# Optimization experiments

Hardware: AMD Instinct MI355X
Metric: run time of the kernel (lower is better)

Reference implementation:

```python
import jax, jax.numpy as jnp
import numpy as np

LAMDA = 0.5

def setup_inputs() -> dict:
    key = jax.random.key(0)
    k1, k2 = jax.random.split(key)
    X_set = jax.random.normal(k1, (8192, 128), dtype=jnp.float32)
    Y_set = jax.random.randint(k2, (8192,), 0, 100, dtype=jnp.int64)
    return {"X_set": X_set, "Y_set": Y_set}

def _pairwise_euclidean(X):
    # X: [N, D] -> D: [N, N] euclidean distances (torch.cdist p=2)
    sq_norms = jnp.sum(X * X, axis=1)  # [N]
    sq = sq_norms[:, None] + sq_norms[None, :] - 2.0 * (X @ X.T)  # [N, N]
    sq = jnp.maximum(sq, 0.0)
    # safe sqrt (zero diagonal) to stay grad-safe under jit
    pos = sq > 0.0
    return jnp.where(pos, jnp.sqrt(jnp.where(pos, sq, 1.0)), 0.0)

def reference(X_set, Y_set):
    X = X_set.reshape(X_set.shape[0], -1)
    D = _pairwise_euclidean(X)  # [N, N]
    same = Y_set[:, None] == Y_set[None, :]  # [N, N] bool
    # Class loop in original == sum of within-class distances (incl. zero diag)
    # minus lamda * sum over all ordered cross-class pairs (each unordered
    # cross pair is counted once for each of its two classes -> full mask).
    pos_sum = jnp.sum(jnp.where(same, D, 0.0))
    neg_sum = jnp.sum(jnp.where(same, 0.0, D))
    return pos_sum - LAMDA * neg_sum
```

## Files before the change

### kernel.cpp

```cpp
#include <hip/hip_runtime.h>

#define N_ROWS 8192
#define DIM    128
#define BM     128
#define NBLK   (N_ROWS / BM)
#define NTRI   (NBLK * (NBLK + 1) / 2)

#define BLOB_PER_RB   65536
#define BLOB_PER_PH   16384

typedef _Float16 half8 __attribute__((ext_vector_type(8)));
typedef float    f32x16 __attribute__((ext_vector_type(16)));

typedef const __attribute__((address_space(1))) unsigned int glb_uint;
typedef __attribute__((address_space(3))) unsigned int lds_uint;

__device__ inline void gload_lds16(const void* g, void* l)
{
    __builtin_amdgcn_global_load_lds((glb_uint*)(uintptr_t)g,
                                     (lds_uint*)(uintptr_t)l, 16, 0, 0);
}

__global__ __launch_bounds__(256)
void prep_tiled(const float* __restrict__ X, char* __restrict__ blob,
                float* __restrict__ norms)
{
    const int t    = blockIdx.x * 256 + threadIdx.x;
    const int ksub = t & 3;
    const int p    = (t >> 2) & 3;
    const int row  = t >> 4;

    const float4* src = (const float4*)(X + (size_t)row * DIM + p * 32 + ksub * 8);
    const float4 v0 = src[0], v1 = src[1];
    const float xs[8] = {v0.x, v0.y, v0.z, v0.w, v1.x, v1.y, v1.z, v1.w};

    half8 h, l;
    float ns = 0.0f;
    #pragma unroll
    for (int i = 0; i < 8; ++i) {
        const float x = xs[i];
        const _Float16 hh = (_Float16)x;
        h[i] = hh;
        l[i] = (_Float16)(x - (float)hh);
        ns = fmaf(x, x, ns);
    }

    const int rb   = row >> 7;
    const int r    = row & 127;
    const int g32  = r >> 5;
    const int q    = ksub >> 1;
    const int slot = (r & 31) + (ksub & 1) * 32;
    char* base = blob + (size_t)rb * BLOB_PER_RB + p * BLOB_PER_PH
               + g32 * 4096 + q * 1024 + slot * 16;
    *(half8*)(base)        = h;
    *(half8*)(base + 2048) = l;

    #pragma unroll
    for (int off = 1; off <= 8; off <<= 1) ns += __shfl_xor(ns, off);
    if ((t & 15) == 0) norms[row] = ns;
}

__global__ __launch_bounds__(256, 4)
void pairsum_mfma(const char* __restrict__ blob, const float* __restrict__ norms,
                  const int* __restrict__ Y, double* __restrict__ gsum)
{
    const int kb = blockIdx.x;
    int bi = (int)((129.0f - sqrtf(fmaf(-8.0f, (float)kb, 129.0f * 129.0f))) * 0.5f);
    while ((bi + 1) * (129 - (bi + 1)) / 2 <= kb) ++bi;
    while (bi * (129 - bi) / 2 > kb) --bi;
    const int bj = bi + (kb - bi * (129 - bi) / 2);
    const int i0 = bi * BM, j0 = bj * BM;

    const int tid  = threadIdx.x;
    const int lane = tid & 63;
    const int w    = tid >> 6;
    const int wy   = w >> 1;
    const int wx   = w & 1;
    const int lr   = lane & 31;
    const int lh   = lane >> 5;

    __shared__ __align__(16) char tile[32768];
    __shared__ float nI[BM], nJ[BM];
    __shared__ int   yI[BM], yJ[BM];
    __shared__ double wsum[4];

    if (tid < BM) { nI[tid] = norms[i0 + tid]; yI[tid] = Y[i0 + tid]; }
    else { const int r = tid & (BM - 1); nJ[r] = norms[j0 + r]; yJ[r] = Y[j0 + r]; }
    __syncthreads();

    const char* Apan = blob + (size_t)bi * BLOB_PER_RB;
    const char* Bpan = blob + (size_t)bj * BLOB_PER_RB;

    f32x16 acc[2][2];
    #pragma unroll
    for (int m = 0; m < 2; ++m)
        #pragma unroll
        for (int n = 0; n < 2; ++n)
            #pragma unroll
            for (int r = 0; r < 16; ++r)
                acc[m][n][r] = 0.0f;

    for (int p = 0; p < 4; ++p) {
        #pragma unroll
        for (int r = 0; r < 4; ++r) {
            gload_lds16(Apan + p * BLOB_PER_PH + r * 4096 + tid * 16,
                        tile + r * 4096 + tid * 16);
            gload_lds16(Bpan + p * BLOB_PER_PH + r * 4096 + tid * 16,
                        tile + 16384 + r * 4096 + tid * 16);
        }
        asm volatile("s_waitcnt vmcnt(0)" ::: "memory");
        __builtin_amdgcn_s_barrier();

        #pragma unroll
        for (int q = 0; q < 2; ++q) {
            half8 ah[2], al[2], bh[2], bl[2];
            #pragma unroll
            for (int m = 0; m < 2; ++m) {
                const int ga = (wy * 2 + m) * 4096 + q * 1024 + lane * 16;
                ah[m] = *(const half8*)(tile + ga);
                al[m] = *(const half8*)(tile + ga + 2048);
                const int gb = 16384 + (wx * 2 + m) * 4096 + q * 1024 + lane * 16;
                bh[m] = *(const half8*)(tile + gb);
                bl[m] = *(const half8*)(tile + gb + 2048);
            }
            #pragma unroll
            for (int m = 0; m < 2; ++m)
                #pragma unroll
                for (int n = 0; n < 2; ++n) {
                    acc[m][n] = __builtin_amdgcn_mfma_f32_32x32x16_f16(ah[m], bh[n], acc[m][n], 0, 0, 0);
                    acc[m][n] = __builtin_amdgcn_mfma_f32_32x32x16_f16(ah[m], bl[n], acc[m][n], 0, 0, 0);
                    acc[m][n] = __builtin_amdgcn_mfma_f32_32x32x16_f16(al[m], bh[n], acc[m][n], 0, 0, 0);
                }
        }
        __builtin_amdgcn_s_barrier();
    }

    float s = 0.0f;
    float nJv[2]; int yJv[2];
    #pragma unroll
    for (int n = 0; n < 2; ++n) {
        const int lj = wx * 64 + n * 32 + lr;
        nJv[n] = nJ[lj]; yJv[n] = yJ[lj];
    }
    #pragma unroll
    for (int m = 0; m < 2; ++m) {
        #pragma unroll
        for (int r = 0; r < 16; ++r) {
            const int rowin = (r & 3) + 8 * (r >> 2) + 4 * lh;
            const int li = wy * 64 + m * 32 + rowin;
            const float ni = nI[li];
            const int   yi = yI[li];
            const int   gi = i0 + li;
            #pragma unroll
            for (int n = 0; n < 2; ++n) {
                const int gj = j0 + wx * 64 + n * 32 + lr;
                float sq = fmaf(-2.0f, acc[m][n][r], ni + nJv[n]);
                sq = fmaxf(sq, 0.0f);
                const float d = __builtin_amdgcn_sqrtf(sq);
                if (gi < gj) s = fmaf((yi == yJv[n]) ? 1.0f : -0.5f, d, s);
            }
        }
    }

    #pragma unroll
    for (int off = 32; off > 0; off >>= 1) s += __shfl_down(s, off);
    if (lane == 0) wsum[w] = (double)s;
    __syncthreads();
    if (tid == 0) atomicAdd(gsum, wsum[0] + wsum[1] + wsum[2] + wsum[3]);
}

__global__ void finalize_kernel(const double* __restrict__ gsum, float* __restrict__ out)
{
    out[0] = (float)(2.0 * gsum[0]);
}

#define LDSPAD 4
#define LDB (BM + LDSPAD)
__global__ __launch_bounds__(256)
void pairsum_valu(const float* __restrict__ X, const int* __restrict__ Y,
                  double* __restrict__ gsum)
{
    const int bj = blockIdx.x, bi = blockIdx.y;
    if (bi > bj) return;
    const int tid = threadIdx.x;
    const int i0 = bi * BM, j0 = bj * BM;
    __shared__ float As[32][LDB], Bs[32][LDB];
    __shared__ float nI[BM], nJ[BM];
    __shared__ int yI[BM], yJ[BM];
    __shared__ double wsum[4];
    {
        const int r = tid & (BM - 1);
        const bool isJ = tid >= BM;
        const int row = (isJ ? j0 : i0) + r;
        const float4* p = (const float4*)(X + (size_t)row * DIM);
        float s = 0.f;
        #pragma unroll
        for (int q = 0; q < DIM / 4; ++q) {
            float4 v = p[q];
            s = fmaf(v.x, v.x, s); s = fmaf(v.y, v.y, s);
            s = fmaf(v.z, v.z, s); s = fmaf(v.w, v.w, s);
        }
        if (isJ) { nJ[r] = s; yJ[r] = Y[row]; }
        else     { nI[r] = s; yI[r] = Y[row]; }
    }
    float dot[8][8];
    #pragma unroll
    for (int m = 0; m < 8; ++m)
        #pragma unroll
        for (int n = 0; n < 8; ++n) dot[m][n] = 0.f;
    const int tx = tid & 15, ty = tid >> 4;
    for (int kc = 0; kc < DIM; kc += 32) {
        __syncthreads();
        #pragma unroll
        for (int p = 0; p < 4; ++p) {
            const int s2 = p * 256 + tid;
            const int row = s2 >> 3, kg = s2 & 7;
            const float4 va = *(const float4*)(X + (size_t)(i0 + row) * DIM + kc + kg * 4);
            const float4 vb = *(const float4*)(X + (size_t)(j0 + row) * DIM + kc + kg * 4);
            As[kg*4+0][row] = va.x; As[kg*4+1][row] = va.y;
            As[kg*4+2][row] = va.z; As[kg*4+3][row] = va.w;
            Bs[kg*4+0][row] = vb.x; Bs[kg*4+1][row] = vb.y;
            Bs[kg*4+2][row] = vb.z; Bs[kg*4+3][row] = vb.w;
        }
        __syncthreads();
        #pragma unroll
        for (int k = 0; k < 32; ++k) {
            float a[8], b[8];
            *(float4*)&a[0] = *(const float4*)&As[k][ty*8];
            *(float4*)&a[4] = *(const float4*)&As[k][ty*8+4];
            *(float4*)&b[0] = *(const float4*)&Bs[k][tx*8];
            *(float4*)&b[4] = *(const float4*)&Bs[k][tx*8+4];
            #pragma unroll
            for (int m = 0; m < 8; ++m)
                #pragma unroll
                for (int n = 0; n < 8; ++n)
                    dot[m][n] = fmaf(a[m], b[n], dot[m][n]);
        }
    }
    float s = 0.f;
    const int ib = ty * 8, jb = tx * 8;
    #pragma unroll
    for (int m = 0; m < 8; ++m) {
        const int gi = i0 + ib + m;
        const float ni = nI[ib + m];
        const int yi = yI[ib + m];
        #pragma unroll
        for (int n = 0; n < 8; ++n) {
            const int gj = j0 + jb + n;
            float sq = fmaf(-2.f, dot[m][n], ni + nJ[jb + n]);
            sq = fmaxf(sq, 0.f);
            const float d = __builtin_amdgcn_sqrtf(sq);
            if (gi < gj) s = fmaf((yi == yJ[jb + n]) ? 1.0f : -0.5f, d, s);
        }
    }
    #pragma unroll
    for (int off = 32; off > 0; off >>= 1) s += __shfl_down(s, off);
    const int lane = tid & 63, wid = tid >> 6;
    if (lane == 0) wsum[wid] = (double)s;
    __syncthreads();
    if (tid == 0) atomicAdd(gsum, wsum[0] + wsum[1] + wsum[2] + wsum[3]);
}

extern "C" void kernel_launch(void* const* d_in, const int* in_sizes, int n_in,
                              void* d_out, int out_size, void* d_ws, size_t ws_size,
                              hipStream_t stream)
{
    const float* X = (const float*)d_in[0];
    const int*   Y = (const int*)d_in[1];
    float* out = (float*)d_out;

    const size_t OFF_BLOB = 64;
    const size_t OFF_NORM = OFF_BLOB + (size_t)NBLK * BLOB_PER_RB;
    const size_t REQ      = OFF_NORM + (size_t)N_ROWS * 4;

    double* gsum = (double*)d_ws;
    hipMemsetAsync(d_ws, 0, sizeof(double), stream);

    if (ws_size >= REQ) {
        char*  blob  = (char*)d_ws + OFF_BLOB;
        float* norms = (float*)((char*)d_ws + OFF_NORM);
        prep_tiled<<<(N_ROWS * 16) / 256, 256, 0, stream>>>(X, blob, norms);
        pairsum_mfma<<<NTRI, 256, 0, stream>>>(blob, norms, Y, gsum);
    } else {
        dim3 grid(NBLK, NBLK);
        pairsum_valu<<<grid, 256, 0, stream>>>(X, Y, gsum);
    }
    finalize_kernel<<<1, 1, 0, stream>>>(gsum, out);
}
```

Measured before the change: 109.2 us.

## Use 256-row tiles with 512-thread blocks and double-buffered LDS K-phases

The MFMA pair-sum kernel now tiles 256x256 row blocks instead of 128x128, using 8 waves per block, each computing a 128x64 sub-tile. The blob layout is re-packed into 8 K-phases of 16 columns, and global-to-LDS loads for the next phase are issued before computing the current one, using two LDS buffers. This halves the number of panel loads per output element and overlaps memory with MFMA. In exchange it uses 64KB of LDS and more accumulator registers, which lowers occupancy, and the triangular grid shrinks to 528 blocks with coarser diagonal waste.

```diff
diff --git a/kernel.cpp b/kernel.cpp
--- a/kernel.cpp
+++ b/kernel.cpp
@@ -1,12 +1,13 @@
 #include <hip/hip_runtime.h>
 
-#define N_ROWS 8192
-#define DIM    128
-#define BM     128
-#define NBLK   (N_ROWS / BM)
-#define NTRI   (NBLK * (NBLK + 1) / 2)
-
-#define BLOB_PER_RB   65536
+#define N_ROWS  8192
+#define DIM     128
+#define BM      256
+#define NPAN    (N_ROWS / BM)
+#define NTRI    (NPAN * (NPAN + 1) / 2)
+#define NPH     8
+
+#define BLOB_PER_RB   131072
 #define BLOB_PER_PH   16384
 
 typedef _Float16 half8 __attribute__((ext_vector_type(8)));
@@ -25,12 +26,13 @@
 void prep_tiled(const float* __restrict__ X, char* __restrict__ blob,
                 float* __restrict__ norms)
 {
-    const int t    = blockIdx.x * 256 + threadIdx.x;
-    const int ksub = t & 3;
-    const int p    = (t >> 2) & 3;
-    const int row  = t >> 4;
-
-    const float4* src = (const float4*)(X + (size_t)row * DIM + p * 32 + ksub * 8);
+    const int t   = blockIdx.x * 256 + threadIdx.x;
+    const int kq  = t & 15;
+    const int p   = kq >> 1;
+    const int ks  = kq & 1;
+    const int row = t >> 4;
+
+    const float4* src = (const float4*)(X + (size_t)row * DIM + kq * 8);
     const float4 v0 = src[0], v1 = src[1];
     const float xs[8] = {v0.x, v0.y, v0.z, v0.w, v1.x, v1.y, v1.z, v1.w};
 
@@ -45,93 +47,105 @@
         ns = fmaf(x, x, ns);
     }
 
-    const int rb   = row >> 7;
-    const int r    = row & 127;
+    const int rb   = row >> 8;
+    const int r    = row & 255;
     const int g32  = r >> 5;
-    const int q    = ksub >> 1;
-    const int slot = (r & 31) + (ksub & 1) * 32;
+    const int slot = (r & 31) + ks * 32;
     char* base = blob + (size_t)rb * BLOB_PER_RB + p * BLOB_PER_PH
-               + g32 * 4096 + q * 1024 + slot * 16;
+               + g32 * 2048 + slot * 16;
     *(half8*)(base)        = h;
-    *(half8*)(base + 2048) = l;
+    *(half8*)(base + 1024) = l;
 
     #pragma unroll
     for (int off = 1; off <= 8; off <<= 1) ns += __shfl_xor(ns, off);
     if ((t & 15) == 0) norms[row] = ns;
 }
 
-__global__ __launch_bounds__(256, 4)
+__global__ __launch_bounds__(512, 2)
 void pairsum_mfma(const char* __restrict__ blob, const float* __restrict__ norms,
                   const int* __restrict__ Y, double* __restrict__ gsum)
 {
     const int kb = blockIdx.x;
-    int bi = (int)((129.0f - sqrtf(fmaf(-8.0f, (float)kb, 129.0f * 129.0f))) * 0.5f);
-    while ((bi + 1) * (129 - (bi + 1)) / 2 <= kb) ++bi;
-    while (bi * (129 - bi) / 2 > kb) --bi;
-    const int bj = bi + (kb - bi * (129 - bi) / 2);
+    int bi = (int)((65.0f - sqrtf(fmaf(-8.0f, (float)kb, 65.0f * 65.0f))) * 0.5f);
+    while ((bi + 1) * (65 - (bi + 1)) / 2 <= kb) ++bi;
+    while (bi * (65 - bi) / 2 > kb) --bi;
+    const int bj = bi + (kb - bi * (65 - bi) / 2);
     const int i0 = bi * BM, j0 = bj * BM;
 
     const int tid  = threadIdx.x;
     const int lane = tid & 63;
     const int w    = tid >> 6;
-    const int wy   = w >> 1;
-    const int wx   = w & 1;
+    const int wy   = w >> 2;
+    const int wx   = w & 3;
     const int lr   = lane & 31;
     const int lh   = lane >> 5;
 
-    __shared__ __align__(16) char tile[32768];
+    __shared__ __align__(16) char tile[65536];
     __shared__ float nI[BM], nJ[BM];
     __shared__ int   yI[BM], yJ[BM];
-    __shared__ double wsum[4];
+    __shared__ double wsum[8];
 
     if (tid < BM) { nI[tid] = norms[i0 + tid]; yI[tid] = Y[i0 + tid]; }
-    else { const int r = tid & (BM - 1); nJ[r] = norms[j0 + r]; yJ[r] = Y[j0 + r]; }
+    else { const int r = tid - BM; nJ[r] = norms[j0 + r]; yJ[r] = Y[j0 + r]; }
     __syncthreads();
 
     const char* Apan = blob + (size_t)bi * BLOB_PER_RB;
     const char* Bpan = blob + (size_t)bj * BLOB_PER_RB;
 
-    f32x16 acc[2][2];
-    #pragma unroll
-    for (int m = 0; m < 2; ++m)
+    auto STAGE = [&](int p, int s) {
+        #pragma unroll
+        for (int r = 0; r < 2; ++r) {
+            gload_lds16(Apan + p * BLOB_PER_PH + r * 8192 + tid * 16,
+                        tile + s * 32768 + r * 8192 + tid * 16);
+            gload_lds16(Bpan + p * BLOB_PER_PH + r * 8192 + tid * 16,
+                        tile + s * 32768 + 16384 + r * 8192 + tid * 16);
+        }
+    };
+
+    f32x16 acc[4][2];
+    #pragma unroll
+    for (int m = 0; m < 4; ++m)
         #pragma unroll
         for (int n = 0; n < 2; ++n)
             #pragma unroll
             for (int r = 0; r < 16; ++r)
                 acc[m][n][r] = 0.0f;
 
-    for (int p = 0; p < 4; ++p) {
-        #pragma unroll
-        for (int r = 0; r < 4; ++r) {
-            gload_lds16(Apan + p * BLOB_PER_PH + r * 4096 + tid * 16,
-                        tile + r * 4096 + tid * 16);
-            gload_lds16(Bpan + p * BLOB_PER_PH + r * 4096 + tid * 16,
-                        tile + 16384 + r * 4096 + tid * 16);
-        }
-        asm volatile("s_waitcnt vmcnt(0)" ::: "memory");
-        __builtin_amdgcn_s_barrier();
-
-        #pragma unroll
-        for (int q = 0; q < 2; ++q) {
-            half8 ah[2], al[2], bh[2], bl[2];
+    STAGE(0, 0);
+    asm volatile("s_waitcnt vmcnt(0)" ::: "memory");
+    __builtin_amdgcn_s_barrier();
+    __builtin_amdgcn_sched_barrier(0);
+
+    #pragma unroll
+    for (int p = 0; p < NPH; ++p) {
+        if (p + 1 < NPH) STAGE(p + 1, (p + 1) & 1);
+
+        const char* Ab = tile + (p & 1) * 32768;
+        const char* Bb = Ab + 16384;
+        half8 ah[4], al[4], bh[2], bl[2];
+        #pragma unroll
+        for (int m = 0; m < 4; ++m) {
+            const int ga = (wy * 4 + m) * 2048 + lane * 16;
+            ah[m] = *(const half8*)(Ab + ga);
+            al[m] = *(const half8*)(Ab + ga + 1024);
+        }
+        #pragma unroll
+        for (int n = 0; n < 2; ++n) {
+            const int gb = (wx * 2 + n) * 2048 + lane * 16;
+            bh[n] = *(const half8*)(Bb + gb);
+            bl[n] = *(const half8*)(Bb + gb + 1024);
+        }
+        #pragma unroll
+        for (int m = 0; m < 4; ++m)
             #pragma unroll
-            for (int m = 0; m < 2; ++m) {
-                const int ga = (wy * 2 + m) * 4096 + q * 1024 + lane * 16;
-                ah[m] = *(const half8*)(tile + ga);
-                al[m] = *(const half8*)(tile + ga + 2048);
-                const int gb = 16384 + (wx * 2 + m) * 4096 + q * 1024 + lane * 16;
-                bh[m] = *(const half8*)(tile + gb);
-                bl[m] = *(const half8*)(tile + gb + 2048);
+            for (int n = 0; n < 2; ++n) {
+                acc[m][n] = __builtin_amdgcn_mfma_f32_32x32x16_f16(ah[m], bh[n], acc[m][n], 0, 0, 0);
+                acc[m][n] = __builtin_amdgcn_mfma_f32_32x32x16_f16(ah[m], bl[n], acc[m][n], 0, 0, 0);
+                acc[m][n] = __builtin_amdgcn_mfma_f32_32x32x16_f16(al[m], bh[n], acc[m][n], 0, 0, 0);
             }
-            #pragma unroll
-            for (int m = 0; m < 2; ++m)
-                #pragma unroll
-                for (int n = 0; n < 2; ++n) {
-                    acc[m][n] = __builtin_amdgcn_mfma_f32_32x32x16_f16(ah[m], bh[n], acc[m][n], 0, 0, 0);
-                    acc[m][n] = __builtin_amdgcn_mfma_f32_32x32x16_f16(ah[m], bl[n], acc[m][n], 0, 0, 0);
-                    acc[m][n] = __builtin_amdgcn_mfma_f32_32x32x16_f16(al[m], bh[n], acc[m][n], 0, 0, 0);
-                }
-        }
+
+        asm volatile("s_waitcnt vmcnt(0) lgkmcnt(0)" ::: "memory");
+        __builtin_amdgcn_sched_barrier(0);
         __builtin_amdgcn_s_barrier();
     }
 
@@ -143,11 +157,11 @@
         nJv[n] = nJ[lj]; yJv[n] = yJ[lj];
     }
     #pragma unroll
-    for (int m = 0; m < 2; ++m) {
+    for (int m = 0; m < 4; ++m) {
         #pragma unroll
         for (int r = 0; r < 16; ++r) {
             const int rowin = (r & 3) + 8 * (r >> 2) + 4 * lh;
-            const int li = wy * 64 + m * 32 + rowin;
+            const int li = wy * 128 + m * 32 + rowin;
             const float ni = nI[li];
             const int   yi = yI[li];
             const int   gi = i0 + li;
@@ -166,7 +180,12 @@
     for (int off = 32; off > 0; off >>= 1) s += __shfl_down(s, off);
     if (lane == 0) wsum[w] = (double)s;
     __syncthreads();
-    if (tid == 0) atomicAdd(gsum, wsum[0] + wsum[1] + wsum[2] + wsum[3]);
+    if (tid == 0) {
+        double t2 = 0.0;
+        #pragma unroll
+        for (int q = 0; q < 8; ++q) t2 += wsum[q];
+        atomicAdd(gsum, t2);
+    }
 }
 
 __global__ void finalize_kernel(const double* __restrict__ gsum, float* __restrict__ out)
@@ -174,8 +193,9 @@
     out[0] = (float)(2.0 * gsum[0]);
 }
 
+#define FBM 128
 #define LDSPAD 4
-#define LDB (BM + LDSPAD)
+#define LDB (FBM + LDSPAD)
 __global__ __launch_bounds__(256)
 void pairsum_valu(const float* __restrict__ X, const int* __restrict__ Y,
                   double* __restrict__ gsum)
@@ -183,14 +203,14 @@
     const int bj = blockIdx.x, bi = blockIdx.y;
     if (bi > bj) return;
     const int tid = threadIdx.x;
-    const int i0 = bi * BM, j0 = bj * BM;
+    const int i0 = bi * FBM, j0 = bj * FBM;
     __shared__ float As[32][LDB], Bs[32][LDB];
-    __shared__ float nI[BM], nJ[BM];
-    __shared__ int yI[BM], yJ[BM];
+    __shared__ float nI[FBM], nJ[FBM];
+    __shared__ int yI[FBM], yJ[FBM];
     __shared__ double wsum[4];
     {
-        const int r = tid & (BM - 1);
-        const bool isJ = tid >= BM;
+        const int r = tid & (FBM - 1);
+        const bool isJ = tid >= FBM;
         const int row = (isJ ? j0 : i0) + r;
         const float4* p = (const float4*)(X + (size_t)row * DIM);
         float s = 0.f;
@@ -270,7 +290,7 @@
     float* out = (float*)d_out;
 
     const size_t OFF_BLOB = 64;
-    const size_t OFF_NORM = OFF_BLOB + (size_t)NBLK * BLOB_PER_RB;
+    const size_t OFF_NORM = OFF_BLOB + (size_t)NPAN * BLOB_PER_RB;
     const size_t REQ      = OFF_NORM + (size_t)N_ROWS * 4;
 
     double* gsum = (double*)d_ws;
@@ -280,9 +300,9 @@
         char*  blob  = (char*)d_ws + OFF_BLOB;
         float* norms = (float*)((char*)d_ws + OFF_NORM);
         prep_tiled<<<(N_ROWS * 16) / 256, 256, 0, stream>>>(X, blob, norms);
-        pairsum_mfma<<<NTRI, 256, 0, stream>>>(blob, norms, Y, gsum);
+        pairsum_mfma<<<NTRI, 512, 0, stream>>>(blob, norms, Y, gsum);
     } else {
-        dim3 grid(NBLK, NBLK);
+        dim3 grid(N_ROWS / FBM, N_ROWS / FBM);
         pairsum_valu<<<grid, 256, 0, stream>>>(X, Y, gsum);
     }
     finalize_kernel<<<1, 1, 0, stream>>>(gsum, out);
```

Result: slower. 113.8 us (+4.2%).

## Drop LDS staging, fold zeroing and finalize into compute kernels

Applied to the files above, without the earlier changes.

The MFMA kernel now reads fragments straight from global memory (the pre-tiled blob) instead of staging panels through LDS with barriers. The memset is moved into the prep kernel, and the finalize launch is replaced by a last-block-done counter pattern. This cuts two launches and all per-phase barriers, at the cost of uncoalesced-ish direct global loads per wave and redundant A/B fetches across waves relying on cache.

```diff
diff --git a/kernel.cpp b/kernel.cpp
--- a/kernel.cpp
+++ b/kernel.cpp
@@ -6,29 +6,24 @@
 #define NBLK   (N_ROWS / BM)
 #define NTRI   (NBLK * (NBLK + 1) / 2)
 
-#define BLOB_PER_RB   65536
-#define BLOB_PER_PH   16384
+#define BLOB_PER_RB 65536
+#define BLOB_PER_PH 16384
 
 typedef _Float16 half8 __attribute__((ext_vector_type(8)));
 typedef float    f32x16 __attribute__((ext_vector_type(16)));
 
-typedef const __attribute__((address_space(1))) unsigned int glb_uint;
-typedef __attribute__((address_space(3))) unsigned int lds_uint;
-
-__device__ inline void gload_lds16(const void* g, void* l)
-{
-    __builtin_amdgcn_global_load_lds((glb_uint*)(uintptr_t)g,
-                                     (lds_uint*)(uintptr_t)l, 16, 0, 0);
-}
-
 __global__ __launch_bounds__(256)
 void prep_tiled(const float* __restrict__ X, char* __restrict__ blob,
-                float* __restrict__ norms)
+                float* __restrict__ norms, double* __restrict__ gsum,
+                unsigned int* __restrict__ counter)
 {
     const int t    = blockIdx.x * 256 + threadIdx.x;
-    const int ksub = t & 3;
-    const int p    = (t >> 2) & 3;
+    const int kq   = t & 15;
+    const int p    = kq >> 2;
+    const int ksub = kq & 3;
     const int row  = t >> 4;
+
+    if (t == 0) { *gsum = 0.0; *counter = 0u; }
 
     const float4* src = (const float4*)(X + (size_t)row * DIM + p * 32 + ksub * 8);
     const float4 v0 = src[0], v1 = src[1];
@@ -47,7 +42,7 @@
 
     const int rb   = row >> 7;
     const int r    = row & 127;
-    const int g32  = r >> 5;
+    const int g32  = (r >> 5) & 3;
     const int q    = ksub >> 1;
     const int slot = (r & 31) + (ksub & 1) * 32;
     char* base = blob + (size_t)rb * BLOB_PER_RB + p * BLOB_PER_PH
@@ -62,7 +57,8 @@
 
 __global__ __launch_bounds__(256, 4)
 void pairsum_mfma(const char* __restrict__ blob, const float* __restrict__ norms,
-                  const int* __restrict__ Y, double* __restrict__ gsum)
+                  const int* __restrict__ Y, double* __restrict__ gsum,
+                  unsigned int* __restrict__ counter, float* __restrict__ out)
 {
     const int kb = blockIdx.x;
     int bi = (int)((129.0f - sqrtf(fmaf(-8.0f, (float)kb, 129.0f * 129.0f))) * 0.5f);
@@ -79,7 +75,6 @@
     const int lr   = lane & 31;
     const int lh   = lane >> 5;
 
-    __shared__ __align__(16) char tile[32768];
     __shared__ float nI[BM], nJ[BM];
     __shared__ int   yI[BM], yJ[BM];
     __shared__ double wsum[4];
@@ -100,28 +95,21 @@
             for (int r = 0; r < 16; ++r)
                 acc[m][n][r] = 0.0f;
 
+    #pragma unroll
     for (int p = 0; p < 4; ++p) {
-        #pragma unroll
-        for (int r = 0; r < 4; ++r) {
-            gload_lds16(Apan + p * BLOB_PER_PH + r * 4096 + tid * 16,
-                        tile + r * 4096 + tid * 16);
-            gload_lds16(Bpan + p * BLOB_PER_PH + r * 4096 + tid * 16,
-                        tile + 16384 + r * 4096 + tid * 16);
-        }
-        asm volatile("s_waitcnt vmcnt(0)" ::: "memory");
-        __builtin_amdgcn_s_barrier();
-
         #pragma unroll
         for (int q = 0; q < 2; ++q) {
             half8 ah[2], al[2], bh[2], bl[2];
             #pragma unroll
             for (int m = 0; m < 2; ++m) {
-                const int ga = (wy * 2 + m) * 4096 + q * 1024 + lane * 16;
-                ah[m] = *(const half8*)(tile + ga);
-                al[m] = *(const half8*)(tile + ga + 2048);
-                const int gb = 16384 + (wx * 2 + m) * 4096 + q * 1024 + lane * 16;
-                bh[m] = *(const half8*)(tile + gb);
-                bl[m] = *(const half8*)(tile + gb + 2048);
+                const char* a = Apan + p * BLOB_PER_PH + (wy * 2 + m) * 4096
+                              + q * 1024 + lane * 16;
+                ah[m] = *(const half8*)a;
+                al[m] = *(const half8*)(a + 2048);
+                const char* b = Bpan + p * BLOB_PER_PH + (wx * 2 + m) * 4096
+                              + q * 1024 + lane * 16;
+                bh[m] = *(const half8*)b;
+                bl[m] = *(const half8*)(b + 2048);
             }
             #pragma unroll
             for (int m = 0; m < 2; ++m)
@@ -132,7 +120,6 @@
                     acc[m][n] = __builtin_amdgcn_mfma_f32_32x32x16_f16(al[m], bh[n], acc[m][n], 0, 0, 0);
                 }
         }
-        __builtin_amdgcn_s_barrier();
     }
 
     float s = 0.0f;
@@ -166,7 +153,16 @@
     for (int off = 32; off > 0; off >>= 1) s += __shfl_down(s, off);
     if (lane == 0) wsum[w] = (double)s;
     __syncthreads();
-    if (tid == 0) atomicAdd(gsum, wsum[0] + wsum[1] + wsum[2] + wsum[3]);
+    if (tid == 0) {
+        atomicAdd(gsum, wsum[0] + wsum[1] + wsum[2] + wsum[3]);
+        __threadfence();
+        const unsigned int old = atomicAdd(counter, 1u);
+        if (old == NTRI - 1) {
+            __threadfence();
+            const double tot = atomicAdd(gsum, 0.0);
+            out[0] = (float)(2.0 * tot);
+        }
+    }
 }
 
 __global__ void finalize_kernel(const double* __restrict__ gsum, float* __restrict__ out)
@@ -273,17 +269,18 @@
     const size_t OFF_NORM = OFF_BLOB + (size_t)NBLK * BLOB_PER_RB;
     const size_t REQ      = OFF_NORM + (size_t)N_ROWS * 4;
 
-    double* gsum = (double*)d_ws;
-    hipMemsetAsync(d_ws, 0, sizeof(double), stream);
+    double*       gsum    = (double*)d_ws;
+    unsigned int* counter = (unsigned int*)((char*)d_ws + 8);
 
     if (ws_size >= REQ) {
         char*  blob  = (char*)d_ws + OFF_BLOB;
         float* norms = (float*)((char*)d_ws + OFF_NORM);
-        prep_tiled<<<(N_ROWS * 16) / 256, 256, 0, stream>>>(X, blob, norms);
-        pairsum_mfma<<<NTRI, 256, 0, stream>>>(blob, norms, Y, gsum);
+        prep_tiled<<<(N_ROWS * 16) / 256, 256, 0, stream>>>(X, blob, norms, gsum, counter);
+        pairsum_mfma<<<NTRI, 256, 0, stream>>>(blob, norms, Y, gsum, counter, out);
     } else {
+        hipMemsetAsync(d_ws, 0, sizeof(double), stream);
         dim3 grid(NBLK, NBLK);
         pairsum_valu<<<grid, 256, 0, stream>>>(X, Y, gsum);
-    }
-    finalize_kernel<<<1, 1, 0, stream>>>(gsum, out);
-}
+        finalize_kernel<<<1, 1, 0, stream>>>(gsum, out);
+    }
+}
```

Measured after the change: 131.7 us. 1.21x slower.
